# Performance work log

Measured on AMD Instinct MI355X. Metric: run time of the kernel, lower is better.

The kernel has to match this reference:

```python
import jax, jax.numpy as jnp
from jax import lax
import numpy as np

B, C, H, W, D = 8, 128, 96, 96, 4  # D must equal 64//16 = 4 (one UAG per depth slice)


def setup_inputs() -> dict:
    key = jax.random.key(0)
    ks = jax.random.split(key, 9)
    s = 0.5 / np.sqrt(C)  # keep the recurrence numerically stable
    def w(k):
        return jax.random.normal(k, (D, C, C), jnp.float32) * s
    def b(k):
        return jax.random.normal(k, (D, C), jnp.float32) * 0.01
    return {
        "x": jax.random.normal(ks[0], (B, C, H, W, D), jnp.float32),
        "W1": w(ks[1]), "b1": b(ks[2]),  # conv1 per-dag weights/bias (kernel_size=1 -> [C,C])
        "W2": w(ks[3]), "b2": b(ks[4]),  # conv2
        "W4": w(ks[5]), "b4": b(ks[6]),  # conv4
        "W5": w(ks[7]), "b5": b(ks[8]),  # conv5
    }


def _dag(xs, w1, bb1, w2, bb2, w4, bb4, w5, bb5):
    # xs: [B,C,H,W]; one UAG_RNN_4Neigh forward.
    def lin(w, bb, v):  # 1x1 Conv1d == channel matmul; v: [B,C,L]
        return jnp.einsum('oc,bcl->bol', w, v) + bb[None, :, None]

    # --- row recurrence (top -> bottom); row 0 passes through unchanged ---
    def row_step(prev, row):
        new = jax.nn.relu(lin(w1, bb1, row) + lin(w2, bb2, prev))
        return new, new

    row0 = xs[:, :, 0, :]                       # [B,C,W]
    rows = jnp.moveaxis(xs[:, :, 1:, :], 2, 0)  # [H-1,B,C,W]
    _, out_rows = lax.scan(row_step, row0, rows)
    hs = jnp.concatenate([row0[None], out_rows], axis=0)  # [H,B,C,W]
    hs = jnp.moveaxis(hs, 0, 2)                            # [B,C,H,W]

    # --- col recurrence (left -> right); col 0 gets relu only ---
    def col_step(prev, col):
        new = jax.nn.relu(lin(w4, bb4, col) + lin(w5, bb5, prev))
        return new, new

    col0 = jax.nn.relu(hs[:, :, :, 0])           # [B,C,H]
    cols = jnp.moveaxis(hs[:, :, :, 1:], 3, 0)   # [W-1,B,C,H]
    _, out_cols = lax.scan(col_step, col0, cols)
    hse = jnp.concatenate([col0[None], out_cols], axis=0)  # [W,B,C,H]
    return jnp.moveaxis(hse, 0, 3)                           # [B,C,H,W]


def reference(x, W1, b1, W2, b2, W4, b4, W5, b5):
    # vmap over the D=4 depth slices, each with its own dag parameters
    hid = jax.vmap(_dag, in_axes=(-1, 0, 0, 0, 0, 0, 0, 0, 0), out_axes=-1)(
        x, W1, b1, W2, b2, W4, b4, W5, b5)
    return x + hid
```

## Files before the change

kernel.cpp:

```cpp
#include <hip/hip_runtime.h>


typedef short bf16x8 __attribute__((ext_vector_type(8)));
typedef float f32x4 __attribute__((ext_vector_type(4)));
typedef unsigned int uint4v __attribute__((ext_vector_type(4)));

__device__ __forceinline__ unsigned short f2bf(float f) {
  unsigned int u = __builtin_bit_cast(unsigned int, f);
  u = (u + 0x7FFFu + ((u >> 16) & 1u)) >> 16;
  return (unsigned short)u;
}
__device__ __forceinline__ float bf2f(unsigned short h) {
  unsigned int u = ((unsigned int)h) << 16;
  return __builtin_bit_cast(float, u);
}

__device__ __forceinline__ int sigma_k(int kap) {
  int kt = kap >> 5, q = (kap >> 3) & 3, j = kap & 7;
  return kt * 32 + ((j >> 2) << 4) + q * 4 + (j & 3);
}

__global__ __launch_bounds__(256) void prep_kernel(
    const float* __restrict__ W1, const float* __restrict__ b1,
    const float* __restrict__ W2, const float* __restrict__ b2,
    const float* __restrict__ W4, const float* __restrict__ b4,
    const float* __restrict__ W5, const float* __restrict__ b5,
    unsigned short* __restrict__ Wb, float* __restrict__ bs12,
    float* __restrict__ bs45) {
  int gid = blockIdx.x * 256 + threadIdx.x;
  if (gid < 4 * 65536) {
    int m = gid >> 16;
    int r = gid & 65535;
    int kap = r & 127;
    int c = sigma_k(kap);
    const float* src = (m == 0) ? W1 : (m == 1) ? W2 : (m == 2) ? W4 : W5;
    Wb[m * 65536 + r] = f2bf(src[(r >> 7) * 128 + c]);
  } else if (gid < 4 * 65536 + 512) {
    int r = gid - 4 * 65536;
    bs12[r] = b1[r] + b2[r];
  } else if (gid < 4 * 65536 + 1024) {
    int r = gid - 4 * 65536 - 512;
    bs45[r] = b4[r] + b5[r];
  }
}

__global__ __launch_bounds__(256) void transpose_kernel(
    const float* __restrict__ x, unsigned short* __restrict__ act) {
  __shared__ unsigned short tile[128 * 208];
  int bid = blockIdx.x;
  int half = bid & 1;
  int rest = bid >> 1;
  int h = rest % 96;
  int b = rest / 96;
  int wd0 = half * 192;
  int tid = threadIdx.x;
#pragma unroll
  for (int it = 0; it < 12; ++it) {
    int cid = it * 256 + tid;
    int c = cid / 24;
    int k = cid % 24;
    const float* xp = x + ((size_t)(b * 128 + c) * 96 + h) * 384 + wd0 + k * 8;
    float4 v0 = *(const float4*)xp;
    float4 v1 = *(const float4*)(xp + 4);
    bf16x8 pk;
    pk[0] = (short)f2bf(v0.x); pk[1] = (short)f2bf(v0.y);
    pk[2] = (short)f2bf(v0.z); pk[3] = (short)f2bf(v0.w);
    pk[4] = (short)f2bf(v1.x); pk[5] = (short)f2bf(v1.y);
    pk[6] = (short)f2bf(v1.z); pk[7] = (short)f2bf(v1.w);
    int ks = k ^ ((c >> 3) & 7);
    *(bf16x8*)&tile[c * 208 + ks * 8] = pk;
  }
  __syncthreads();
#pragma unroll
  for (int it = 0; it < 12; ++it) {
    int sid = it * 256 + tid;
    int wdl = sid >> 4;
    int cc = sid & 15;
    int k = wdl >> 3, off = wdl & 7;
    int ktq = cc >> 2, qq = cc & 3;
    bf16x8 pk;
#pragma unroll
    for (int j = 0; j < 8; ++j) {
      int c = ktq * 32 + ((j >> 2) << 4) + qq * 4 + (j & 3);
      int ks = k ^ ((c >> 3) & 7);
      pk[j] = (short)tile[c * 208 + ks * 8 + off];
    }
    int wdg = wd0 + wdl;
    int d = wdg & 3, w = wdg >> 2;
    *(bf16x8*)(act + ((((size_t)(b * 4 + d) * 96 + h) * 96 + w) * 128 + cc * 8)) = pk;
  }
}

#define SCAN_STEP(CUR, NXT, BN, PF)                                            \
  do {                                                                         \
    _Pragma("unroll") for (int kt = 0; kt < 4; ++kt)                           \
      _Pragma("unroll") for (int mi = 0; mi < 8; ++mi)                         \
        CUR[mi] = __builtin_amdgcn_mfma_f32_16x16x32_bf16(A2[mi][kt], Bp[kt],  \
                                                          CUR[mi], 0, 0, 0);   \
    _Pragma("unroll") for (int kt = 0; kt < 4; ++kt) {                         \
      unsigned int u0, u1, u2, u3;                                             \
      float a0 = fmaxf(CUR[2 * kt][0], 0.f);                                   \
      float a1 = fmaxf(CUR[2 * kt][1], 0.f);                                   \
      float a2 = fmaxf(CUR[2 * kt][2], 0.f);                                   \
      float a3 = fmaxf(CUR[2 * kt][3], 0.f);                                   \
      float c0 = fmaxf(CUR[2 * kt + 1][0], 0.f);                               \
      float c1 = fmaxf(CUR[2 * kt + 1][1], 0.f);                               \
      float c2 = fmaxf(CUR[2 * kt + 1][2], 0.f);                               \
      float c3 = fmaxf(CUR[2 * kt + 1][3], 0.f);                               \
      asm("v_cvt_pk_bf16_f32 %0, %1, %2" : "=v"(u0) : "v"(a0), "v"(a1));       \
      asm("v_cvt_pk_bf16_f32 %0, %1, %2" : "=v"(u1) : "v"(a2), "v"(a3));       \
      asm("v_cvt_pk_bf16_f32 %0, %1, %2" : "=v"(u2) : "v"(c0), "v"(c1));       \
      asm("v_cvt_pk_bf16_f32 %0, %1, %2" : "=v"(u3) : "v"(c2), "v"(c3));       \
      uint4v uu;                                                               \
      uu[0] = u0; uu[1] = u1; uu[2] = u2; uu[3] = u3;                          \
      Bp[kt] = __builtin_bit_cast(bf16x8, uu);                                 \
      *(bf16x8*)(outrow + kt * 32) = Bp[kt];                                   \
    }                                                                          \
    _Pragma("unroll") for (int mi = 0; mi < 8; ++mi)                           \
      NXT[mi] = __builtin_amdgcn_mfma_f32_16x16x32_bf16(A1[mi][0], BN[0],      \
                                                        bias[mi], 0, 0, 0);    \
    _Pragma("unroll") for (int kt = 1; kt < 4; ++kt)                           \
      _Pragma("unroll") for (int mi = 0; mi < 8; ++mi)                         \
        NXT[mi] = __builtin_amdgcn_mfma_f32_16x16x32_bf16(A1[mi][kt], BN[kt],  \
                                                          NXT[mi], 0, 0, 0);   \
    _Pragma("unroll") for (int kt = 0; kt < 4; ++kt)                           \
      BN[kt] = *(const bf16x8*)(PF + kt * 32);                                 \
    outrow += OUT_STRIDE;                                                      \
  } while (0)

__global__ __launch_bounds__(64, 1) void row_kernel(
    unsigned short* act, const unsigned short* __restrict__ Wb,
    const float* __restrict__ bs12) {
  int bid = blockIdx.x;
  int wt = bid % 6;
  int bd = bid / 6;
  int d = bd & 3;
  int w0 = wt * 16;
  int lane = threadIdx.x & 63;
  int q = lane >> 4;
  int n = lane & 15;

  const unsigned short* w1p = Wb + d * 16384;
  const unsigned short* w2p = Wb + 65536 + d * 16384;

  bf16x8 A1[8][4], A2[8][4];
#pragma unroll
  for (int mi = 0; mi < 8; ++mi) {
    int c = mi * 16 + n;
#pragma unroll
    for (int kt = 0; kt < 4; ++kt) {
      int k0 = kt * 32 + q * 8;
      A1[mi][kt] = *(const bf16x8*)(w1p + c * 128 + k0);
      A2[mi][kt] = *(const bf16x8*)(w2p + c * 128 + k0);
    }
  }
  f32x4 bias[8];
#pragma unroll
  for (int mi = 0; mi < 8; ++mi)
#pragma unroll
    for (int r = 0; r < 4; ++r)
      bias[mi][r] = bs12[d * 128 + mi * 16 + q * 4 + r];

  size_t base = ((size_t)bd * 9216 + (size_t)(w0 + n)) * 128 + q * 8;
  const unsigned short* xrow = act + base;
  unsigned short* outrow = act + base + 12288;
  const int OUT_STRIDE = 12288;

  bf16x8 Bp[4], Bn_[4], Bf_[4];
#pragma unroll
  for (int kt = 0; kt < 4; ++kt)
    Bp[kt] = *(const bf16x8*)(xrow + kt * 32);

  f32x4 accA_[8], accB_[8];
#pragma unroll
  for (int kt = 0; kt < 4; ++kt)
    Bn_[kt] = *(const bf16x8*)(xrow + 12288 + kt * 32);
#pragma unroll
  for (int mi = 0; mi < 8; ++mi)
    accA_[mi] = __builtin_amdgcn_mfma_f32_16x16x32_bf16(A1[mi][0], Bn_[0],
                                                        bias[mi], 0, 0, 0);
#pragma unroll
  for (int kt = 1; kt < 4; ++kt)
#pragma unroll
    for (int mi = 0; mi < 8; ++mi)
      accA_[mi] = __builtin_amdgcn_mfma_f32_16x16x32_bf16(A1[mi][kt], Bn_[kt],
                                                          accA_[mi], 0, 0, 0);
#pragma unroll
  for (int kt = 0; kt < 4; ++kt) {
    Bn_[kt] = *(const bf16x8*)(xrow + 2 * 12288 + kt * 32);
    Bf_[kt] = *(const bf16x8*)(xrow + 3 * 12288 + kt * 32);
  }

#pragma unroll 1
  for (int h = 1; h <= 93; h += 2) {
    const unsigned short* pf1 =
        xrow + (size_t)(h + 3 <= 95 ? h + 3 : 95) * 12288;
    SCAN_STEP(accA_, accB_, Bn_, pf1);
    const unsigned short* pf2 =
        xrow + (size_t)(h + 4 <= 95 ? h + 4 : 95) * 12288;
    SCAN_STEP(accB_, accA_, Bf_, pf2);
  }
  {
    const unsigned short* pf3 = xrow + (size_t)95 * 12288;
    SCAN_STEP(accA_, accB_, Bn_, pf3);
  }
}

__global__ __launch_bounds__(64, 1) void col_kernel(
    unsigned short* act, const unsigned short* __restrict__ Wb,
    const float* __restrict__ bs45) {
  int bid = blockIdx.x;
  int ht = bid % 6;
  int bd = bid / 6;
  int d = bd & 3;
  int h0 = ht * 16;
  int lane = threadIdx.x & 63;
  int q = lane >> 4;
  int n = lane & 15;

  const unsigned short* w4p = Wb + 2 * 65536 + d * 16384;
  const unsigned short* w5p = Wb + 3 * 65536 + d * 16384;

  bf16x8 A1[8][4], A2[8][4];
#pragma unroll
  for (int mi = 0; mi < 8; ++mi) {
    int c = mi * 16 + n;
#pragma unroll
    for (int kt = 0; kt < 4; ++kt) {
      int k0 = kt * 32 + q * 8;
      A1[mi][kt] = *(const bf16x8*)(w4p + c * 128 + k0);
      A2[mi][kt] = *(const bf16x8*)(w5p + c * 128 + k0);
    }
  }
  f32x4 bias[8];
#pragma unroll
  for (int mi = 0; mi < 8; ++mi)
#pragma unroll
    for (int r = 0; r < 4; ++r)
      bias[mi][r] = bs45[d * 128 + mi * 16 + q * 4 + r];

  size_t base = ((size_t)bd * 9216 + (size_t)(h0 + n) * 96) * 128 + q * 8;
  const unsigned short* ccol = act + base;
  unsigned short* outrow = act + base;
  const int OUT_STRIDE = 128;

  bf16x8 Bp[4], Bn_[4], Bf_[4];
#pragma unroll
  for (int kt = 0; kt < 4; ++kt) {
    bf16x8 v = *(const bf16x8*)(ccol + kt * 32);
#pragma unroll
    for (int j = 0; j < 8; ++j) {
      unsigned short uv = (unsigned short)v[j];
      if (uv & 0x8000u) v[j] = 0;
    }
    Bp[kt] = v;
    *(bf16x8*)(outrow + kt * 32) = v;
  }
  outrow += 128;

  f32x4 accA_[8], accB_[8];
#pragma unroll
  for (int kt = 0; kt < 4; ++kt)
    Bn_[kt] = *(const bf16x8*)(ccol + 128 + kt * 32);
#pragma unroll
  for (int mi = 0; mi < 8; ++mi)
    accA_[mi] = __builtin_amdgcn_mfma_f32_16x16x32_bf16(A1[mi][0], Bn_[0],
                                                        bias[mi], 0, 0, 0);
#pragma unroll
  for (int kt = 1; kt < 4; ++kt)
#pragma unroll
    for (int mi = 0; mi < 8; ++mi)
      accA_[mi] = __builtin_amdgcn_mfma_f32_16x16x32_bf16(A1[mi][kt], Bn_[kt],
                                                          accA_[mi], 0, 0, 0);
#pragma unroll
  for (int kt = 0; kt < 4; ++kt) {
    Bn_[kt] = *(const bf16x8*)(ccol + 2 * 128 + kt * 32);
    Bf_[kt] = *(const bf16x8*)(ccol + 3 * 128 + kt * 32);
  }

#pragma unroll 1
  for (int w = 1; w <= 93; w += 2) {
    const unsigned short* pf1 = ccol + (size_t)(w + 3 <= 95 ? w + 3 : 95) * 128;
    SCAN_STEP(accA_, accB_, Bn_, pf1);
    const unsigned short* pf2 = ccol + (size_t)(w + 4 <= 95 ? w + 4 : 95) * 128;
    SCAN_STEP(accB_, accA_, Bf_, pf2);
  }
  {
    const unsigned short* pf3 = ccol + (size_t)95 * 128;
    SCAN_STEP(accA_, accB_, Bn_, pf3);
  }
}

__global__ __launch_bounds__(256) void out_kernel(
    const float* __restrict__ x, const unsigned short* __restrict__ act,
    float* __restrict__ out) {
  __shared__ unsigned short tile[128 * 208];
  int bid = blockIdx.x;
  int half = bid & 1;
  int rest = bid >> 1;
  int h = rest % 96;
  int b = rest / 96;
  int wd0 = half * 192;
  int tid = threadIdx.x;
#pragma unroll
  for (int it = 0; it < 12; ++it) {
    int gid = it * 256 + tid;
    int wdl = gid >> 4;
    int cc = gid & 15;
    int wdg = wd0 + wdl;
    int d = wdg & 3, w = wdg >> 2;
    bf16x8 v = *(const bf16x8*)(
        act + ((((size_t)(b * 4 + d) * 96 + h) * 96 + w) * 128 + cc * 8));
    int k = wdl >> 3, off = wdl & 7;
    int ktq = cc >> 2, qq = cc & 3;
#pragma unroll
    for (int j = 0; j < 8; ++j) {
      int c = ktq * 32 + ((j >> 2) << 4) + qq * 4 + (j & 3);
      int ks = k ^ ((c >> 3) & 7);
      tile[c * 208 + ks * 8 + off] = (unsigned short)v[j];
    }
  }
  __syncthreads();
#pragma unroll
  for (int it = 0; it < 12; ++it) {
    int sid = it * 256 + tid;
    int c = sid / 24;
    int k = sid % 24;
    int ks = k ^ ((c >> 3) & 7);
    bf16x8 pk = *(const bf16x8*)&tile[c * 208 + ks * 8];
    size_t o = ((size_t)(b * 128 + c) * 96 + h) * 384 + wd0 + k * 8;
    float4 a0 = *(const float4*)(x + o);
    float4 a1 = *(const float4*)(x + o + 4);
    float4 r0, r1;
    r0.x = a0.x + bf2f((unsigned short)pk[0]);
    r0.y = a0.y + bf2f((unsigned short)pk[1]);
    r0.z = a0.z + bf2f((unsigned short)pk[2]);
    r0.w = a0.w + bf2f((unsigned short)pk[3]);
    r1.x = a1.x + bf2f((unsigned short)pk[4]);
    r1.y = a1.y + bf2f((unsigned short)pk[5]);
    r1.z = a1.z + bf2f((unsigned short)pk[6]);
    r1.w = a1.w + bf2f((unsigned short)pk[7]);
    *(float4*)(out + o) = r0;
    *(float4*)(out + o + 4) = r1;
  }
}

extern "C" void kernel_launch(void* const* d_in, const int* in_sizes, int n_in,
                              void* d_out, int out_size, void* d_ws,
                              size_t ws_size, hipStream_t stream) {
  (void)in_sizes; (void)n_in; (void)out_size; (void)ws_size;
  const float* x  = (const float*)d_in[0];
  const float* W1 = (const float*)d_in[1];
  const float* b1 = (const float*)d_in[2];
  const float* W2 = (const float*)d_in[3];
  const float* b2 = (const float*)d_in[4];
  const float* W4 = (const float*)d_in[5];
  const float* b4 = (const float*)d_in[6];
  const float* W5 = (const float*)d_in[7];
  const float* b5 = (const float*)d_in[8];
  float* out = (float*)d_out;

  char* ws = (char*)d_ws;
  unsigned short* Wb  = (unsigned short*)(ws);
  float* bs12         = (float*)(ws + 524288);
  float* bs45         = (float*)(ws + 526336);
  unsigned short* act = (unsigned short*)(ws + 528384);

  prep_kernel<<<(4 * 65536 + 1024 + 255) / 256, 256, 0, stream>>>(
      W1, b1, W2, b2, W4, b4, W5, b5, Wb, bs12, bs45);
  transpose_kernel<<<8 * 96 * 2, 256, 0, stream>>>(x, act);
  row_kernel<<<192, 64, 0, stream>>>(act, Wb, bs12);
  col_kernel<<<192, 64, 0, stream>>>(act, Wb, bs45);
  out_kernel<<<8 * 96 * 2, 256, 0, stream>>>(x, act, out);
}
```

Before: 518.7 us.

## Split recurrence into producer/consumer waves with LDS ring buffer

Each scan block now runs two waves: one computes the non-recurrent input projection plus bias for upcoming steps and stores accumulators into a 4-slot LDS ring, the other adds the recurrent matmul, applies ReLU and writes outputs. Flags in shared memory with sleep-polling coordinate the two waves. This shortens the serial dependency chain per step by moving half the MFMAs off the critical path, at the cost of LDS traffic, spin-wait latency and reliance on LDS ordering between waves.

```diff
diff --git a/kernel.cpp b/kernel.cpp
--- a/kernel.cpp
+++ b/kernel.cpp
@@ -91,203 +91,278 @@
   }
 }
 
-#define SCAN_STEP(CUR, NXT, BN, PF)                                            \
-  do {                                                                         \
-    _Pragma("unroll") for (int kt = 0; kt < 4; ++kt)                           \
-      _Pragma("unroll") for (int mi = 0; mi < 8; ++mi)                         \
-        CUR[mi] = __builtin_amdgcn_mfma_f32_16x16x32_bf16(A2[mi][kt], Bp[kt],  \
-                                                          CUR[mi], 0, 0, 0);   \
-    _Pragma("unroll") for (int kt = 0; kt < 4; ++kt) {                         \
-      unsigned int u0, u1, u2, u3;                                             \
-      float a0 = fmaxf(CUR[2 * kt][0], 0.f);                                   \
-      float a1 = fmaxf(CUR[2 * kt][1], 0.f);                                   \
-      float a2 = fmaxf(CUR[2 * kt][2], 0.f);                                   \
-      float a3 = fmaxf(CUR[2 * kt][3], 0.f);                                   \
-      float c0 = fmaxf(CUR[2 * kt + 1][0], 0.f);                               \
-      float c1 = fmaxf(CUR[2 * kt + 1][1], 0.f);                               \
-      float c2 = fmaxf(CUR[2 * kt + 1][2], 0.f);                               \
-      float c3 = fmaxf(CUR[2 * kt + 1][3], 0.f);                               \
-      asm("v_cvt_pk_bf16_f32 %0, %1, %2" : "=v"(u0) : "v"(a0), "v"(a1));       \
-      asm("v_cvt_pk_bf16_f32 %0, %1, %2" : "=v"(u1) : "v"(a2), "v"(a3));       \
-      asm("v_cvt_pk_bf16_f32 %0, %1, %2" : "=v"(u2) : "v"(c0), "v"(c1));       \
-      asm("v_cvt_pk_bf16_f32 %0, %1, %2" : "=v"(u3) : "v"(c2), "v"(c3));       \
-      uint4v uu;                                                               \
-      uu[0] = u0; uu[1] = u1; uu[2] = u2; uu[3] = u3;                          \
-      Bp[kt] = __builtin_bit_cast(bf16x8, uu);                                 \
-      *(bf16x8*)(outrow + kt * 32) = Bp[kt];                                   \
-    }                                                                          \
-    _Pragma("unroll") for (int mi = 0; mi < 8; ++mi)                           \
-      NXT[mi] = __builtin_amdgcn_mfma_f32_16x16x32_bf16(A1[mi][0], BN[0],      \
-                                                        bias[mi], 0, 0, 0);    \
-    _Pragma("unroll") for (int kt = 1; kt < 4; ++kt)                           \
-      _Pragma("unroll") for (int mi = 0; mi < 8; ++mi)                         \
-        NXT[mi] = __builtin_amdgcn_mfma_f32_16x16x32_bf16(A1[mi][kt], BN[kt],  \
-                                                          NXT[mi], 0, 0, 0);   \
-    _Pragma("unroll") for (int kt = 0; kt < 4; ++kt)                           \
-      BN[kt] = *(const bf16x8*)(PF + kt * 32);                                 \
-    outrow += OUT_STRIDE;                                                      \
-  } while (0)
-
-__global__ __launch_bounds__(64, 1) void row_kernel(
+__global__ __launch_bounds__(128) void row_kernel(
     unsigned short* act, const unsigned short* __restrict__ Wb,
     const float* __restrict__ bs12) {
+  __shared__ float slots[4][8][64][4];
+  __shared__ int flags[64];
   int bid = blockIdx.x;
   int wt = bid % 6;
   int bd = bid / 6;
   int d = bd & 3;
   int w0 = wt * 16;
-  int lane = threadIdx.x & 63;
+  int tid = threadIdx.x;
+  int wave = tid >> 6;
+  int lane = tid & 63;
   int q = lane >> 4;
   int n = lane & 15;
-
-  const unsigned short* w1p = Wb + d * 16384;
-  const unsigned short* w2p = Wb + 65536 + d * 16384;
-
-  bf16x8 A1[8][4], A2[8][4];
-#pragma unroll
-  for (int mi = 0; mi < 8; ++mi) {
-    int c = mi * 16 + n;
+  volatile int* fprod = &flags[0];
+  volatile int* fcons = &flags[32];
+  if (tid < 2) flags[tid * 32] = 0;
+  __syncthreads();
+
+  size_t bd9216 = (size_t)bd * 9216;
+  size_t base = (bd9216 + (size_t)(w0 + n)) * 128 + q * 8;
+
+  if (wave == 1) {
+    const unsigned short* w1p = Wb + d * 16384;
+    bf16x8 A1[8][4];
+#pragma unroll
+    for (int mi = 0; mi < 8; ++mi) {
+      int c = mi * 16 + n;
+#pragma unroll
+      for (int kt = 0; kt < 4; ++kt)
+        A1[mi][kt] = *(const bf16x8*)(w1p + c * 128 + kt * 32 + q * 8);
+    }
+    f32x4 bias[8];
+#pragma unroll
+    for (int mi = 0; mi < 8; ++mi)
+#pragma unroll
+      for (int r = 0; r < 4; ++r)
+        bias[mi][r] = bs12[d * 128 + mi * 16 + q * 4 + r];
+    const unsigned short* xrow = act + base;
+    bf16x8 Bn[4], Bf[4];
 #pragma unroll
     for (int kt = 0; kt < 4; ++kt) {
-      int k0 = kt * 32 + q * 8;
-      A1[mi][kt] = *(const bf16x8*)(w1p + c * 128 + k0);
-      A2[mi][kt] = *(const bf16x8*)(w2p + c * 128 + k0);
-    }
-  }
-  f32x4 bias[8];
-#pragma unroll
-  for (int mi = 0; mi < 8; ++mi)
-#pragma unroll
-    for (int r = 0; r < 4; ++r)
-      bias[mi][r] = bs12[d * 128 + mi * 16 + q * 4 + r];
-
-  size_t base = ((size_t)bd * 9216 + (size_t)(w0 + n)) * 128 + q * 8;
-  const unsigned short* xrow = act + base;
-  unsigned short* outrow = act + base + 12288;
-  const int OUT_STRIDE = 12288;
-
-  bf16x8 Bp[4], Bn_[4], Bf_[4];
-#pragma unroll
-  for (int kt = 0; kt < 4; ++kt)
-    Bp[kt] = *(const bf16x8*)(xrow + kt * 32);
-
-  f32x4 accA_[8], accB_[8];
-#pragma unroll
-  for (int kt = 0; kt < 4; ++kt)
-    Bn_[kt] = *(const bf16x8*)(xrow + 12288 + kt * 32);
-#pragma unroll
-  for (int mi = 0; mi < 8; ++mi)
-    accA_[mi] = __builtin_amdgcn_mfma_f32_16x16x32_bf16(A1[mi][0], Bn_[0],
-                                                        bias[mi], 0, 0, 0);
-#pragma unroll
-  for (int kt = 1; kt < 4; ++kt)
-#pragma unroll
-    for (int mi = 0; mi < 8; ++mi)
-      accA_[mi] = __builtin_amdgcn_mfma_f32_16x16x32_bf16(A1[mi][kt], Bn_[kt],
-                                                          accA_[mi], 0, 0, 0);
-#pragma unroll
-  for (int kt = 0; kt < 4; ++kt) {
-    Bn_[kt] = *(const bf16x8*)(xrow + 2 * 12288 + kt * 32);
-    Bf_[kt] = *(const bf16x8*)(xrow + 3 * 12288 + kt * 32);
-  }
-
+      Bn[kt] = *(const bf16x8*)(xrow + (size_t)1 * 12288 + kt * 32);
+      Bf[kt] = *(const bf16x8*)(xrow + (size_t)2 * 12288 + kt * 32);
+    }
 #pragma unroll 1
-  for (int h = 1; h <= 93; h += 2) {
-    const unsigned short* pf1 =
-        xrow + (size_t)(h + 3 <= 95 ? h + 3 : 95) * 12288;
-    SCAN_STEP(accA_, accB_, Bn_, pf1);
-    const unsigned short* pf2 =
-        xrow + (size_t)(h + 4 <= 95 ? h + 4 : 95) * 12288;
-    SCAN_STEP(accB_, accA_, Bf_, pf2);
-  }
-  {
-    const unsigned short* pf3 = xrow + (size_t)95 * 12288;
-    SCAN_STEP(accA_, accB_, Bn_, pf3);
-  }
-}
-
-__global__ __launch_bounds__(64, 1) void col_kernel(
+    for (int h = 1; h <= 95; ++h) {
+      while (h - *fcons > 3) __builtin_amdgcn_s_sleep(1);
+      asm volatile("" ::: "memory");
+      f32x4 acc[8];
+#pragma unroll
+      for (int mi = 0; mi < 8; ++mi)
+        acc[mi] = __builtin_amdgcn_mfma_f32_16x16x32_bf16(A1[mi][0], Bn[0],
+                                                          bias[mi], 0, 0, 0);
+#pragma unroll
+      for (int kt = 1; kt < 4; ++kt)
+#pragma unroll
+        for (int mi = 0; mi < 8; ++mi)
+          acc[mi] = __builtin_amdgcn_mfma_f32_16x16x32_bf16(A1[mi][kt], Bn[kt],
+                                                            acc[mi], 0, 0, 0);
+      int hp = (h + 2 <= 95) ? h + 2 : 95;
+      const unsigned short* pf = xrow + (size_t)hp * 12288;
+#pragma unroll
+      for (int kt = 0; kt < 4; ++kt) {
+        Bn[kt] = Bf[kt];
+        Bf[kt] = *(const bf16x8*)(pf + kt * 32);
+      }
+      float* sp = &slots[h & 3][0][lane][0];
+#pragma unroll
+      for (int mi = 0; mi < 8; ++mi)
+        *(f32x4*)(sp + mi * 256) = acc[mi];
+      asm volatile("s_waitcnt lgkmcnt(0)" ::: "memory");
+      if (lane == 0) *fprod = h;
+    }
+  } else {
+    const unsigned short* w2p = Wb + 65536 + d * 16384;
+    bf16x8 A2[8][4];
+#pragma unroll
+    for (int mi = 0; mi < 8; ++mi) {
+      int c = mi * 16 + n;
+#pragma unroll
+      for (int kt = 0; kt < 4; ++kt)
+        A2[mi][kt] = *(const bf16x8*)(w2p + c * 128 + kt * 32 + q * 8);
+    }
+    const unsigned short* xrow = act + base;
+    unsigned short* outrow = act + base + 12288;
+    bf16x8 Bp[4];
+#pragma unroll
+    for (int kt = 0; kt < 4; ++kt)
+      Bp[kt] = *(const bf16x8*)(xrow + kt * 32);
+#pragma unroll 1
+    for (int h = 1; h <= 95; ++h) {
+      while (*fprod < h) __builtin_amdgcn_s_sleep(1);
+      asm volatile("" ::: "memory");
+      const float* sp = &slots[h & 3][0][lane][0];
+      f32x4 acc[8];
+#pragma unroll
+      for (int mi = 0; mi < 8; ++mi)
+        acc[mi] = *(const f32x4*)(sp + mi * 256);
+#pragma unroll
+      for (int kt = 0; kt < 4; ++kt)
+#pragma unroll
+        for (int mi = 0; mi < 8; ++mi)
+          acc[mi] = __builtin_amdgcn_mfma_f32_16x16x32_bf16(A2[mi][kt], Bp[kt],
+                                                            acc[mi], 0, 0, 0);
+#pragma unroll
+      for (int kt = 0; kt < 4; ++kt) {
+        unsigned int u0, u1, u2, u3;
+        float a0 = fmaxf(acc[2 * kt][0], 0.f);
+        float a1 = fmaxf(acc[2 * kt][1], 0.f);
+        float a2 = fmaxf(acc[2 * kt][2], 0.f);
+        float a3 = fmaxf(acc[2 * kt][3], 0.f);
+        float c0 = fmaxf(acc[2 * kt + 1][0], 0.f);
+        float c1 = fmaxf(acc[2 * kt + 1][1], 0.f);
+        float c2 = fmaxf(acc[2 * kt + 1][2], 0.f);
+        float c3 = fmaxf(acc[2 * kt + 1][3], 0.f);
+        asm("v_cvt_pk_bf16_f32 %0, %1, %2" : "=v"(u0) : "v"(a0), "v"(a1));
+        asm("v_cvt_pk_bf16_f32 %0, %1, %2" : "=v"(u1) : "v"(a2), "v"(a3));
+        asm("v_cvt_pk_bf16_f32 %0, %1, %2" : "=v"(u2) : "v"(c0), "v"(c1));
+        asm("v_cvt_pk_bf16_f32 %0, %1, %2" : "=v"(u3) : "v"(c2), "v"(c3));
+        uint4v uu;
+        uu[0] = u0; uu[1] = u1; uu[2] = u2; uu[3] = u3;
+        Bp[kt] = __builtin_bit_cast(bf16x8, uu);
+        *(bf16x8*)(outrow + kt * 32) = Bp[kt];
+      }
+      outrow += 12288;
+      asm volatile("" ::: "memory");
+      if (lane == 0) *fcons = h;
+    }
+  }
+}
+
+__global__ __launch_bounds__(128) void col_kernel(
     unsigned short* act, const unsigned short* __restrict__ Wb,
     const float* __restrict__ bs45) {
+  __shared__ float slots[4][8][64][4];
+  __shared__ int flags[64];
   int bid = blockIdx.x;
   int ht = bid % 6;
   int bd = bid / 6;
   int d = bd & 3;
   int h0 = ht * 16;
-  int lane = threadIdx.x & 63;
+  int tid = threadIdx.x;
+  int wave = tid >> 6;
+  int lane = tid & 63;
   int q = lane >> 4;
   int n = lane & 15;
-
-  const unsigned short* w4p = Wb + 2 * 65536 + d * 16384;
-  const unsigned short* w5p = Wb + 3 * 65536 + d * 16384;
-
-  bf16x8 A1[8][4], A2[8][4];
-#pragma unroll
-  for (int mi = 0; mi < 8; ++mi) {
-    int c = mi * 16 + n;
+  volatile int* fprod = &flags[0];
+  volatile int* fcons = &flags[32];
+  if (tid < 2) flags[tid * 32] = 0;
+  __syncthreads();
+
+  size_t bd9216 = (size_t)bd * 9216;
+  size_t base = (bd9216 + (size_t)(h0 + n) * 96) * 128 + q * 8;
+
+  if (wave == 1) {
+    const unsigned short* w4p = Wb + 2 * 65536 + d * 16384;
+    bf16x8 A1[8][4];
+#pragma unroll
+    for (int mi = 0; mi < 8; ++mi) {
+      int c = mi * 16 + n;
+#pragma unroll
+      for (int kt = 0; kt < 4; ++kt)
+        A1[mi][kt] = *(const bf16x8*)(w4p + c * 128 + kt * 32 + q * 8);
+    }
+    f32x4 bias[8];
+#pragma unroll
+    for (int mi = 0; mi < 8; ++mi)
+#pragma unroll
+      for (int r = 0; r < 4; ++r)
+        bias[mi][r] = bs45[d * 128 + mi * 16 + q * 4 + r];
+    const unsigned short* ccol = act + base;
+    bf16x8 Bn[4], Bf[4];
 #pragma unroll
     for (int kt = 0; kt < 4; ++kt) {
-      int k0 = kt * 32 + q * 8;
-      A1[mi][kt] = *(const bf16x8*)(w4p + c * 128 + k0);
-      A2[mi][kt] = *(const bf16x8*)(w5p + c * 128 + k0);
-    }
-  }
-  f32x4 bias[8];
-#pragma unroll
-  for (int mi = 0; mi < 8; ++mi)
-#pragma unroll
-    for (int r = 0; r < 4; ++r)
-      bias[mi][r] = bs45[d * 128 + mi * 16 + q * 4 + r];
-
-  size_t base = ((size_t)bd * 9216 + (size_t)(h0 + n) * 96) * 128 + q * 8;
-  const unsigned short* ccol = act + base;
-  unsigned short* outrow = act + base;
-  const int OUT_STRIDE = 128;
-
-  bf16x8 Bp[4], Bn_[4], Bf_[4];
-#pragma unroll
-  for (int kt = 0; kt < 4; ++kt) {
-    bf16x8 v = *(const bf16x8*)(ccol + kt * 32);
-#pragma unroll
-    for (int j = 0; j < 8; ++j) {
-      unsigned short uv = (unsigned short)v[j];
-      if (uv & 0x8000u) v[j] = 0;
-    }
-    Bp[kt] = v;
-    *(bf16x8*)(outrow + kt * 32) = v;
-  }
-  outrow += 128;
-
-  f32x4 accA_[8], accB_[8];
-#pragma unroll
-  for (int kt = 0; kt < 4; ++kt)
-    Bn_[kt] = *(const bf16x8*)(ccol + 128 + kt * 32);
-#pragma unroll
-  for (int mi = 0; mi < 8; ++mi)
-    accA_[mi] = __builtin_amdgcn_mfma_f32_16x16x32_bf16(A1[mi][0], Bn_[0],
-                                                        bias[mi], 0, 0, 0);
-#pragma unroll
-  for (int kt = 1; kt < 4; ++kt)
-#pragma unroll
-    for (int mi = 0; mi < 8; ++mi)
-      accA_[mi] = __builtin_amdgcn_mfma_f32_16x16x32_bf16(A1[mi][kt], Bn_[kt],
-                                                          accA_[mi], 0, 0, 0);
-#pragma unroll
-  for (int kt = 0; kt < 4; ++kt) {
-    Bn_[kt] = *(const bf16x8*)(ccol + 2 * 128 + kt * 32);
-    Bf_[kt] = *(const bf16x8*)(ccol + 3 * 128 + kt * 32);
-  }
-
+      Bn[kt] = *(const bf16x8*)(ccol + (size_t)1 * 128 + kt * 32);
+      Bf[kt] = *(const bf16x8*)(ccol + (size_t)2 * 128 + kt * 32);
+    }
 #pragma unroll 1
-  for (int w = 1; w <= 93; w += 2) {
-    const unsigned short* pf1 = ccol + (size_t)(w + 3 <= 95 ? w + 3 : 95) * 128;
-    SCAN_STEP(accA_, accB_, Bn_, pf1);
-    const unsigned short* pf2 = ccol + (size_t)(w + 4 <= 95 ? w + 4 : 95) * 128;
-    SCAN_STEP(accB_, accA_, Bf_, pf2);
-  }
-  {
-    const unsigned short* pf3 = ccol + (size_t)95 * 128;
-    SCAN_STEP(accA_, accB_, Bn_, pf3);
+    for (int w = 1; w <= 95; ++w) {
+      while (w - *fcons > 3) __builtin_amdgcn_s_sleep(1);
+      asm volatile("" ::: "memory");
+      f32x4 acc[8];
+#pragma unroll
+      for (int mi = 0; mi < 8; ++mi)
+        acc[mi] = __builtin_amdgcn_mfma_f32_16x16x32_bf16(A1[mi][0], Bn[0],
+                                                          bias[mi], 0, 0, 0);
+#pragma unroll
+      for (int kt = 1; kt < 4; ++kt)
+#pragma unroll
+        for (int mi = 0; mi < 8; ++mi)
+          acc[mi] = __builtin_amdgcn_mfma_f32_16x16x32_bf16(A1[mi][kt], Bn[kt],
+                                                            acc[mi], 0, 0, 0);
+      int wp = (w + 2 <= 95) ? w + 2 : 95;
+      const unsigned short* pf = ccol + (size_t)wp * 128;
+#pragma unroll
+      for (int kt = 0; kt < 4; ++kt) {
+        Bn[kt] = Bf[kt];
+        Bf[kt] = *(const bf16x8*)(pf + kt * 32);
+      }
+      float* sp = &slots[w & 3][0][lane][0];
+#pragma unroll
+      for (int mi = 0; mi < 8; ++mi)
+        *(f32x4*)(sp + mi * 256) = acc[mi];
+      asm volatile("s_waitcnt lgkmcnt(0)" ::: "memory");
+      if (lane == 0) *fprod = w;
+    }
+  } else {
+    const unsigned short* w5p = Wb + 3 * 65536 + d * 16384;
+    bf16x8 A2[8][4];
+#pragma unroll
+    for (int mi = 0; mi < 8; ++mi) {
+      int c = mi * 16 + n;
+#pragma unroll
+      for (int kt = 0; kt < 4; ++kt)
+        A2[mi][kt] = *(const bf16x8*)(w5p + c * 128 + kt * 32 + q * 8);
+    }
+    const unsigned short* ccol = act + base;
+    unsigned short* outrow = act + base;
+    bf16x8 Bp[4];
+#pragma unroll
+    for (int kt = 0; kt < 4; ++kt) {
+      bf16x8 v = *(const bf16x8*)(ccol + kt * 32);
+#pragma unroll
+      for (int j = 0; j < 8; ++j) {
+        unsigned short uv = (unsigned short)v[j];
+        if (uv & 0x8000u) v[j] = 0;
+      }
+      Bp[kt] = v;
+      *(bf16x8*)(outrow + kt * 32) = v;
+    }
+    outrow += 128;
+#pragma unroll 1
+    for (int w = 1; w <= 95; ++w) {
+      while (*fprod < w) __builtin_amdgcn_s_sleep(1);
+      asm volatile("" ::: "memory");
+      const float* sp = &slots[w & 3][0][lane][0];
+      f32x4 acc[8];
+#pragma unroll
+      for (int mi = 0; mi < 8; ++mi)
+        acc[mi] = *(const f32x4*)(sp + mi * 256);
+#pragma unroll
+      for (int kt = 0; kt < 4; ++kt)
+#pragma unroll
+        for (int mi = 0; mi < 8; ++mi)
+          acc[mi] = __builtin_amdgcn_mfma_f32_16x16x32_bf16(A2[mi][kt], Bp[kt],
+                                                            acc[mi], 0, 0, 0);
+#pragma unroll
+      for (int kt = 0; kt < 4; ++kt) {
+        unsigned int u0, u1, u2, u3;
+        float a0 = fmaxf(acc[2 * kt][0], 0.f);
+        float a1 = fmaxf(acc[2 * kt][1], 0.f);
+        float a2 = fmaxf(acc[2 * kt][2], 0.f);
+        float a3 = fmaxf(acc[2 * kt][3], 0.f);
+        float c0 = fmaxf(acc[2 * kt + 1][0], 0.f);
+        float c1 = fmaxf(acc[2 * kt + 1][1], 0.f);
+        float c2 = fmaxf(acc[2 * kt + 1][2], 0.f);
+        float c3 = fmaxf(acc[2 * kt + 1][3], 0.f);
+        asm("v_cvt_pk_bf16_f32 %0, %1, %2" : "=v"(u0) : "v"(a0), "v"(a1));
+        asm("v_cvt_pk_bf16_f32 %0, %1, %2" : "=v"(u1) : "v"(a2), "v"(a3));
+        asm("v_cvt_pk_bf16_f32 %0, %1, %2" : "=v"(u2) : "v"(c0), "v"(c1));
+        asm("v_cvt_pk_bf16_f32 %0, %1, %2" : "=v"(u3) : "v"(c2), "v"(c3));
+        uint4v uu;
+        uu[0] = u0; uu[1] = u1; uu[2] = u2; uu[3] = u3;
+        Bp[kt] = __builtin_bit_cast(bf16x8, uu);
+        *(bf16x8*)(outrow + kt * 32) = Bp[kt];
+      }
+      outrow += 128;
+      asm volatile("" ::: "memory");
+      if (lane == 0) *fcons = w;
+    }
   }
 }
 
@@ -369,7 +444,7 @@
   prep_kernel<<<(4 * 65536 + 1024 + 255) / 256, 256, 0, stream>>>(
       W1, b1, W2, b2, W4, b4, W5, b5, Wb, bs12, bs45);
   transpose_kernel<<<8 * 96 * 2, 256, 0, stream>>>(x, act);
-  row_kernel<<<192, 64, 0, stream>>>(act, Wb, bs12);
-  col_kernel<<<192, 64, 0, stream>>>(act, Wb, bs45);
+  row_kernel<<<192, 128, 0, stream>>>(act, Wb, bs12);
+  col_kernel<<<192, 128, 0, stream>>>(act, Wb, bs45);
   out_kernel<<<8 * 96 * 2, 256, 0, stream>>>(x, act, out);
 }
```

After: 474.8 us. 1.09x faster.

## Split scan across four warp-specialized wavefronts with LDS flag handoff

Applied to the files above, without the earlier changes.

The row and column scans now run four wavefronts per block instead of one. Two producer waves compute the input-projection term (W1/W4 times x plus bias) ahead of time into LDS slots. Two consumer waves each own half of the output channels, exchange their halves of the previous hidden state through LDS, and apply the recurrent matmul, ReLU and bf16 store. The aim is to take the input projection off the serial critical path and halve the recurrent MFMA work per wave, at the cost of spin-wait flag synchronisation and LDS round-trips on every step.

```diff
diff --git a/kernel.cpp b/kernel.cpp
--- a/kernel.cpp
+++ b/kernel.cpp
@@ -91,44 +91,171 @@
   }
 }
 
-#define SCAN_STEP(CUR, NXT, BN, PF)                                            \
-  do {                                                                         \
-    _Pragma("unroll") for (int kt = 0; kt < 4; ++kt)                           \
-      _Pragma("unroll") for (int mi = 0; mi < 8; ++mi)                         \
-        CUR[mi] = __builtin_amdgcn_mfma_f32_16x16x32_bf16(A2[mi][kt], Bp[kt],  \
-                                                          CUR[mi], 0, 0, 0);   \
-    _Pragma("unroll") for (int kt = 0; kt < 4; ++kt) {                         \
-      unsigned int u0, u1, u2, u3;                                             \
-      float a0 = fmaxf(CUR[2 * kt][0], 0.f);                                   \
-      float a1 = fmaxf(CUR[2 * kt][1], 0.f);                                   \
-      float a2 = fmaxf(CUR[2 * kt][2], 0.f);                                   \
-      float a3 = fmaxf(CUR[2 * kt][3], 0.f);                                   \
-      float c0 = fmaxf(CUR[2 * kt + 1][0], 0.f);                               \
-      float c1 = fmaxf(CUR[2 * kt + 1][1], 0.f);                               \
-      float c2 = fmaxf(CUR[2 * kt + 1][2], 0.f);                               \
-      float c3 = fmaxf(CUR[2 * kt + 1][3], 0.f);                               \
-      asm("v_cvt_pk_bf16_f32 %0, %1, %2" : "=v"(u0) : "v"(a0), "v"(a1));       \
-      asm("v_cvt_pk_bf16_f32 %0, %1, %2" : "=v"(u1) : "v"(a2), "v"(a3));       \
-      asm("v_cvt_pk_bf16_f32 %0, %1, %2" : "=v"(u2) : "v"(c0), "v"(c1));       \
-      asm("v_cvt_pk_bf16_f32 %0, %1, %2" : "=v"(u3) : "v"(c2), "v"(c3));       \
-      uint4v uu;                                                               \
-      uu[0] = u0; uu[1] = u1; uu[2] = u2; uu[3] = u3;                          \
-      Bp[kt] = __builtin_bit_cast(bf16x8, uu);                                 \
-      *(bf16x8*)(outrow + kt * 32) = Bp[kt];                                   \
-    }                                                                          \
-    _Pragma("unroll") for (int mi = 0; mi < 8; ++mi)                           \
-      NXT[mi] = __builtin_amdgcn_mfma_f32_16x16x32_bf16(A1[mi][0], BN[0],      \
-                                                        bias[mi], 0, 0, 0);    \
-    _Pragma("unroll") for (int kt = 1; kt < 4; ++kt)                           \
-      _Pragma("unroll") for (int mi = 0; mi < 8; ++mi)                         \
-        NXT[mi] = __builtin_amdgcn_mfma_f32_16x16x32_bf16(A1[mi][kt], BN[kt],  \
-                                                          NXT[mi], 0, 0, 0);   \
-    _Pragma("unroll") for (int kt = 0; kt < 4; ++kt)                           \
-      BN[kt] = *(const bf16x8*)(PF + kt * 32);                                 \
-    outrow += OUT_STRIDE;                                                      \
-  } while (0)
-
-__global__ __launch_bounds__(64, 1) void row_kernel(
+#define FPW(s) F[(0 + (s)) * 16]
+#define FPC(s) F[(2 + (s)) * 16]
+#define FXW(s) F[(4 + (s)) * 16]
+#define FXR(s) F[(6 + (s)) * 16]
+
+template <int STRIDE, bool SEED_RELU>
+__device__ __forceinline__ void scan_body(
+    unsigned short* act, const unsigned short* wfp, const unsigned short* wrp,
+    const float* bsum, size_t base, int d) {
+  __shared__ float pslot[2][2][4][64][4];
+  __shared__ unsigned short xpart[2][2][2][512];
+  __shared__ int flg[8][16];
+  volatile int* F = &flg[0][0];
+  int tid = threadIdx.x;
+  int wv = tid >> 6;
+  int lane = tid & 63;
+  int q = lane >> 4, n = lane & 15;
+  int s = wv & 1;
+
+  if (tid < 8) flg[tid][0] = (tid >= 6) ? -1 : 0;
+
+  const unsigned short* inp = act + base;
+
+  if (wv >= 2) {
+    bf16x8 A1[4][4];
+#pragma unroll
+    for (int mi = 0; mi < 4; ++mi) {
+      int c = (4 * s + mi) * 16 + n;
+#pragma unroll
+      for (int kt = 0; kt < 4; ++kt)
+        A1[mi][kt] = *(const bf16x8*)(wfp + c * 128 + kt * 32 + q * 8);
+    }
+    f32x4 bias[4];
+#pragma unroll
+    for (int mi = 0; mi < 4; ++mi)
+#pragma unroll
+      for (int r = 0; r < 4; ++r)
+        bias[mi][r] = bsum[d * 128 + (4 * s + mi) * 16 + q * 4 + r];
+    bf16x8 Bn[4], Bf[4];
+#pragma unroll
+    for (int kt = 0; kt < 4; ++kt) {
+      Bn[kt] = *(const bf16x8*)(inp + (size_t)1 * STRIDE + kt * 32);
+      Bf[kt] = *(const bf16x8*)(inp + (size_t)2 * STRIDE + kt * 32);
+    }
+    __syncthreads();
+#pragma unroll 1
+    for (int t = 1; t <= 95; ++t) {
+      while (t - FPC(s) > 2) {}
+      asm volatile("" ::: "memory");
+      f32x4 acc[4];
+#pragma unroll
+      for (int mi = 0; mi < 4; ++mi)
+        acc[mi] = __builtin_amdgcn_mfma_f32_16x16x32_bf16(A1[mi][0], Bn[0],
+                                                          bias[mi], 0, 0, 0);
+#pragma unroll
+      for (int kt = 1; kt < 4; ++kt)
+#pragma unroll
+        for (int mi = 0; mi < 4; ++mi)
+          acc[mi] = __builtin_amdgcn_mfma_f32_16x16x32_bf16(A1[mi][kt], Bn[kt],
+                                                            acc[mi], 0, 0, 0);
+      int tp = (t + 2 <= 95) ? t + 2 : 95;
+      const unsigned short* pf = inp + (size_t)tp * STRIDE;
+#pragma unroll
+      for (int kt = 0; kt < 4; ++kt) {
+        Bn[kt] = Bf[kt];
+        Bf[kt] = *(const bf16x8*)(pf + kt * 32);
+      }
+      float* sp = &pslot[s][t & 1][0][lane][0];
+#pragma unroll
+      for (int mi = 0; mi < 4; ++mi)
+        *(f32x4*)(sp + mi * 256) = acc[mi];
+      asm volatile("s_waitcnt lgkmcnt(0)" ::: "memory");
+      if (lane == 0) FPW(s) = t;
+    }
+  } else {
+    bf16x8 A2[4][4];
+#pragma unroll
+    for (int mi = 0; mi < 4; ++mi) {
+      int c = (4 * s + mi) * 16 + n;
+#pragma unroll
+      for (int kt = 0; kt < 4; ++kt)
+        A2[mi][kt] = *(const bf16x8*)(wrp + c * 128 + kt * 32 + q * 8);
+    }
+    unsigned short* outp = act + base;
+    bf16x8 Bo[2];
+#pragma unroll
+    for (int ktl = 0; ktl < 2; ++ktl) {
+      bf16x8 v = *(const bf16x8*)(inp + (2 * s + ktl) * 32);
+      if (SEED_RELU) {
+#pragma unroll
+        for (int j = 0; j < 8; ++j) {
+          unsigned short uv = (unsigned short)v[j];
+          if (uv & 0x8000u) v[j] = 0;
+        }
+        *(bf16x8*)(outp + (2 * s + ktl) * 32) = v;
+      }
+      Bo[ktl] = v;
+      *(bf16x8*)&xpart[0][s][ktl][lane * 8] = v;
+    }
+    if (SEED_RELU) outp += STRIDE;
+    else outp += STRIDE;
+    __syncthreads();
+#pragma unroll 1
+    for (int t = 1; t <= 95; ++t) {
+      while (FXW(1 - s) < t - 1) {}
+      asm volatile("" ::: "memory");
+      const unsigned short* xp0 = &xpart[(t - 1) & 1][1 - s][0][lane * 8];
+      bf16x8 Bq0 = *(const bf16x8*)xp0;
+      bf16x8 Bq1 = *(const bf16x8*)(xp0 + 512);
+      while (FPW(s) < t) {}
+      asm volatile("" ::: "memory");
+      const float* sp = &pslot[s][t & 1][0][lane][0];
+      f32x4 acc[4];
+#pragma unroll
+      for (int mi = 0; mi < 4; ++mi)
+        acc[mi] = *(const f32x4*)(sp + mi * 256);
+      asm volatile("s_waitcnt lgkmcnt(0)" ::: "memory");
+      if (lane == 0) { FPC(s) = t; FXR(s) = t - 1; }
+#pragma unroll
+      for (int ktl = 0; ktl < 2; ++ktl)
+#pragma unroll
+        for (int mi = 0; mi < 4; ++mi)
+          acc[mi] = __builtin_amdgcn_mfma_f32_16x16x32_bf16(
+              A2[mi][2 * s + ktl], Bo[ktl], acc[mi], 0, 0, 0);
+#pragma unroll
+      for (int mi = 0; mi < 4; ++mi)
+        acc[mi] = __builtin_amdgcn_mfma_f32_16x16x32_bf16(
+            A2[mi][2 * (1 - s) + 0], Bq0, acc[mi], 0, 0, 0);
+#pragma unroll
+      for (int mi = 0; mi < 4; ++mi)
+        acc[mi] = __builtin_amdgcn_mfma_f32_16x16x32_bf16(
+            A2[mi][2 * (1 - s) + 1], Bq1, acc[mi], 0, 0, 0);
+#pragma unroll
+      for (int ktl = 0; ktl < 2; ++ktl) {
+        unsigned int u0, u1, u2, u3;
+        float a0 = fmaxf(acc[2 * ktl][0], 0.f);
+        float a1 = fmaxf(acc[2 * ktl][1], 0.f);
+        float a2 = fmaxf(acc[2 * ktl][2], 0.f);
+        float a3 = fmaxf(acc[2 * ktl][3], 0.f);
+        float c0 = fmaxf(acc[2 * ktl + 1][0], 0.f);
+        float c1 = fmaxf(acc[2 * ktl + 1][1], 0.f);
+        float c2 = fmaxf(acc[2 * ktl + 1][2], 0.f);
+        float c3 = fmaxf(acc[2 * ktl + 1][3], 0.f);
+        asm("v_cvt_pk_bf16_f32 %0, %1, %2" : "=v"(u0) : "v"(a0), "v"(a1));
+        asm("v_cvt_pk_bf16_f32 %0, %1, %2" : "=v"(u1) : "v"(a2), "v"(a3));
+        asm("v_cvt_pk_bf16_f32 %0, %1, %2" : "=v"(u2) : "v"(c0), "v"(c1));
+        asm("v_cvt_pk_bf16_f32 %0, %1, %2" : "=v"(u3) : "v"(c2), "v"(c3));
+        uint4v uu;
+        uu[0] = u0; uu[1] = u1; uu[2] = u2; uu[3] = u3;
+        Bo[ktl] = __builtin_bit_cast(bf16x8, uu);
+        *(bf16x8*)(outp + (2 * s + ktl) * 32) = Bo[ktl];
+      }
+      outp += STRIDE;
+      while (FXR(1 - s) < t - 2) {}
+      asm volatile("" ::: "memory");
+      unsigned short* xw = &xpart[t & 1][s][0][lane * 8];
+      *(bf16x8*)xw = Bo[0];
+      *(bf16x8*)(xw + 512) = Bo[1];
+      asm volatile("s_waitcnt lgkmcnt(0)" ::: "memory");
+      if (lane == 0) FXW(s) = t;
+    }
+  }
+}
+
+__global__ __launch_bounds__(256, 1) void row_kernel(
     unsigned short* act, const unsigned short* __restrict__ Wb,
     const float* __restrict__ bs12) {
   int bid = blockIdx.x;
@@ -137,76 +264,13 @@
   int d = bd & 3;
   int w0 = wt * 16;
   int lane = threadIdx.x & 63;
-  int q = lane >> 4;
-  int n = lane & 15;
-
-  const unsigned short* w1p = Wb + d * 16384;
-  const unsigned short* w2p = Wb + 65536 + d * 16384;
-
-  bf16x8 A1[8][4], A2[8][4];
-#pragma unroll
-  for (int mi = 0; mi < 8; ++mi) {
-    int c = mi * 16 + n;
-#pragma unroll
-    for (int kt = 0; kt < 4; ++kt) {
-      int k0 = kt * 32 + q * 8;
-      A1[mi][kt] = *(const bf16x8*)(w1p + c * 128 + k0);
-      A2[mi][kt] = *(const bf16x8*)(w2p + c * 128 + k0);
-    }
-  }
-  f32x4 bias[8];
-#pragma unroll
-  for (int mi = 0; mi < 8; ++mi)
-#pragma unroll
-    for (int r = 0; r < 4; ++r)
-      bias[mi][r] = bs12[d * 128 + mi * 16 + q * 4 + r];
-
+  int q = lane >> 4, n = lane & 15;
   size_t base = ((size_t)bd * 9216 + (size_t)(w0 + n)) * 128 + q * 8;
-  const unsigned short* xrow = act + base;
-  unsigned short* outrow = act + base + 12288;
-  const int OUT_STRIDE = 12288;
-
-  bf16x8 Bp[4], Bn_[4], Bf_[4];
-#pragma unroll
-  for (int kt = 0; kt < 4; ++kt)
-    Bp[kt] = *(const bf16x8*)(xrow + kt * 32);
-
-  f32x4 accA_[8], accB_[8];
-#pragma unroll
-  for (int kt = 0; kt < 4; ++kt)
-    Bn_[kt] = *(const bf16x8*)(xrow + 12288 + kt * 32);
-#pragma unroll
-  for (int mi = 0; mi < 8; ++mi)
-    accA_[mi] = __builtin_amdgcn_mfma_f32_16x16x32_bf16(A1[mi][0], Bn_[0],
-                                                        bias[mi], 0, 0, 0);
-#pragma unroll
-  for (int kt = 1; kt < 4; ++kt)
-#pragma unroll
-    for (int mi = 0; mi < 8; ++mi)
-      accA_[mi] = __builtin_amdgcn_mfma_f32_16x16x32_bf16(A1[mi][kt], Bn_[kt],
-                                                          accA_[mi], 0, 0, 0);
-#pragma unroll
-  for (int kt = 0; kt < 4; ++kt) {
-    Bn_[kt] = *(const bf16x8*)(xrow + 2 * 12288 + kt * 32);
-    Bf_[kt] = *(const bf16x8*)(xrow + 3 * 12288 + kt * 32);
-  }
-
-#pragma unroll 1
-  for (int h = 1; h <= 93; h += 2) {
-    const unsigned short* pf1 =
-        xrow + (size_t)(h + 3 <= 95 ? h + 3 : 95) * 12288;
-    SCAN_STEP(accA_, accB_, Bn_, pf1);
-    const unsigned short* pf2 =
-        xrow + (size_t)(h + 4 <= 95 ? h + 4 : 95) * 12288;
-    SCAN_STEP(accB_, accA_, Bf_, pf2);
-  }
-  {
-    const unsigned short* pf3 = xrow + (size_t)95 * 12288;
-    SCAN_STEP(accA_, accB_, Bn_, pf3);
-  }
-}
-
-__global__ __launch_bounds__(64, 1) void col_kernel(
+  scan_body<12288, false>(act, Wb + d * 16384, Wb + 65536 + d * 16384, bs12,
+                          base, d);
+}
+
+__global__ __launch_bounds__(256, 1) void col_kernel(
     unsigned short* act, const unsigned short* __restrict__ Wb,
     const float* __restrict__ bs45) {
   int bid = blockIdx.x;
@@ -215,80 +279,10 @@
   int d = bd & 3;
   int h0 = ht * 16;
   int lane = threadIdx.x & 63;
-  int q = lane >> 4;
-  int n = lane & 15;
-
-  const unsigned short* w4p = Wb + 2 * 65536 + d * 16384;
-  const unsigned short* w5p = Wb + 3 * 65536 + d * 16384;
-
-  bf16x8 A1[8][4], A2[8][4];
-#pragma unroll
-  for (int mi = 0; mi < 8; ++mi) {
-    int c = mi * 16 + n;
-#pragma unroll
-    for (int kt = 0; kt < 4; ++kt) {
-      int k0 = kt * 32 + q * 8;
-      A1[mi][kt] = *(const bf16x8*)(w4p + c * 128 + k0);
-      A2[mi][kt] = *(const bf16x8*)(w5p + c * 128 + k0);
-    }
-  }
-  f32x4 bias[8];
-#pragma unroll
-  for (int mi = 0; mi < 8; ++mi)
-#pragma unroll
-    for (int r = 0; r < 4; ++r)
-      bias[mi][r] = bs45[d * 128 + mi * 16 + q * 4 + r];
-
+  int q = lane >> 4, n = lane & 15;
   size_t base = ((size_t)bd * 9216 + (size_t)(h0 + n) * 96) * 128 + q * 8;
-  const unsigned short* ccol = act + base;
-  unsigned short* outrow = act + base;
-  const int OUT_STRIDE = 128;
-
-  bf16x8 Bp[4], Bn_[4], Bf_[4];
-#pragma unroll
-  for (int kt = 0; kt < 4; ++kt) {
-    bf16x8 v = *(const bf16x8*)(ccol + kt * 32);
-#pragma unroll
-    for (int j = 0; j < 8; ++j) {
-      unsigned short uv = (unsigned short)v[j];
-      if (uv & 0x8000u) v[j] = 0;
-    }
-    Bp[kt] = v;
-    *(bf16x8*)(outrow + kt * 32) = v;
-  }
-  outrow += 128;
-
-  f32x4 accA_[8], accB_[8];
-#pragma unroll
-  for (int kt = 0; kt < 4; ++kt)
-    Bn_[kt] = *(const bf16x8*)(ccol + 128 + kt * 32);
-#pragma unroll
-  for (int mi = 0; mi < 8; ++mi)
-    accA_[mi] = __builtin_amdgcn_mfma_f32_16x16x32_bf16(A1[mi][0], Bn_[0],
-                                                        bias[mi], 0, 0, 0);
-#pragma unroll
-  for (int kt = 1; kt < 4; ++kt)
-#pragma unroll
-    for (int mi = 0; mi < 8; ++mi)
-      accA_[mi] = __builtin_amdgcn_mfma_f32_16x16x32_bf16(A1[mi][kt], Bn_[kt],
-                                                          accA_[mi], 0, 0, 0);
-#pragma unroll
-  for (int kt = 0; kt < 4; ++kt) {
-    Bn_[kt] = *(const bf16x8*)(ccol + 2 * 128 + kt * 32);
-    Bf_[kt] = *(const bf16x8*)(ccol + 3 * 128 + kt * 32);
-  }
-
-#pragma unroll 1
-  for (int w = 1; w <= 93; w += 2) {
-    const unsigned short* pf1 = ccol + (size_t)(w + 3 <= 95 ? w + 3 : 95) * 128;
-    SCAN_STEP(accA_, accB_, Bn_, pf1);
-    const unsigned short* pf2 = ccol + (size_t)(w + 4 <= 95 ? w + 4 : 95) * 128;
-    SCAN_STEP(accB_, accA_, Bf_, pf2);
-  }
-  {
-    const unsigned short* pf3 = ccol + (size_t)95 * 128;
-    SCAN_STEP(accA_, accB_, Bn_, pf3);
-  }
+  scan_body<128, true>(act, Wb + 2 * 65536 + d * 16384,
+                       Wb + 3 * 65536 + d * 16384, bs45, base, d);
 }
 
 __global__ __launch_bounds__(256) void out_kernel(
@@ -369,7 +363,7 @@
   prep_kernel<<<(4 * 65536 + 1024 + 255) / 256, 256, 0, stream>>>(
       W1, b1, W2, b2, W4, b4, W5, b5, Wb, bs12, bs45);
   transpose_kernel<<<8 * 96 * 2, 256, 0, stream>>>(x, act);
-  row_kernel<<<192, 64, 0, stream>>>(act, Wb, bs12);
-  col_kernel<<<192, 64, 0, stream>>>(act, Wb, bs45);
+  row_kernel<<<192, 256, 0, stream>>>(act, Wb, bs12);
+  col_kernel<<<192, 256, 0, stream>>>(act, Wb, bs45);
   out_kernel<<<8 * 96 * 2, 256, 0, stream>>>(x, act, out);
 }
```

Result: slower. 705.8 us (+36.1%).
